# Performance work log

Hardware: AMD Instinct MI355X
Metric: run time of the kernel (lower is better)

Reference implementation:

```python
import jax, jax.numpy as jnp
import numpy as np

B, S, DIM = 2, 2048, 2048
H, KV = 16, 8
HD = DIM // H          # 128 head_dim
N_REP = H // KV        # 2


def _rope(x, cos, sin):
    # x: (B,S,h,HD) with interleaved (real, imag) pairs along last dim
    xr = x[..., 0::2]                      # (B,S,h,HD/2)
    xi = x[..., 1::2]
    cos = cos[None, :, None, :]            # (1,S,1,HD/2)
    sin = sin[None, :, None, :]
    or_ = xr * cos - xi * sin
    oi_ = xr * sin + xi * cos
    return jnp.stack([or_, oi_], axis=-1).reshape(x.shape)


def setup_inputs() -> dict:
    key = jax.random.key(0)
    ks = jax.random.split(key, 5)
    x = jax.random.normal(ks[0], (B, S, DIM), dtype=jnp.float32)
    # RoPE tables: theta = 10000, half = HD/2
    inv_freq = 1.0 / (10000.0 ** (np.arange(0, HD, 2, dtype=np.float32) / HD))
    t = np.arange(S, dtype=np.float32)
    ang = np.outer(t, inv_freq)                           # (S, HD/2)
    freqs_cos = jnp.asarray(np.cos(ang), dtype=jnp.float32)
    freqs_sin = jnp.asarray(np.sin(ang), dtype=jnp.float32)
    sc = 0.02
    wq = jax.random.normal(ks[1], (DIM, H * HD), dtype=jnp.float32) * sc
    wk = jax.random.normal(ks[2], (DIM, KV * HD), dtype=jnp.float32) * sc
    wv = jax.random.normal(ks[3], (DIM, KV * HD), dtype=jnp.float32) * sc
    wo = jax.random.normal(ks[4], (DIM, DIM), dtype=jnp.float32) * sc
    return {"x": x, "freqs_cos": freqs_cos, "freqs_sin": freqs_sin,
            "wq": wq, "wk": wk, "wv": wv, "wo": wo}


def reference(x, freqs_cos, freqs_sin, wq, wk, wv, wo):
    b, s, _ = x.shape
    xq = (x @ wq).reshape(b, s, H, HD)
    xk = (x @ wk).reshape(b, s, KV, HD)
    xv = (x @ wv).reshape(b, s, KV, HD)
    xq = _rope(xq, freqs_cos, freqs_sin)
    xk = _rope(xk, freqs_cos, freqs_sin)
    # GQA: repeat kv heads n_rep times along head axis
    xk = jnp.repeat(xk, N_REP, axis=2)     # (b,s,H,HD)
    xv = jnp.repeat(xv, N_REP, axis=2)
    scores = jnp.einsum('bqhd,bkhd->bhqk', xq, xk) / jnp.sqrt(
        jnp.asarray(HD, dtype=x.dtype))
    mask = jnp.triu(jnp.full((s, s), -jnp.inf, dtype=x.dtype), k=1)
    attn = jax.nn.softmax(scores + mask[None, None, :, :], axis=-1)
    out = jnp.einsum('bhqk,bkhd->bqhd', attn, xv).reshape(b, s, DIM)
    return out @ wo
```

## Files before the change

kernel.cpp:

```cpp
#include <hip/hip_runtime.h>

typedef unsigned short u16;
typedef short bf16x8 __attribute__((ext_vector_type(8)));
typedef float f32x4 __attribute__((ext_vector_type(4)));
typedef unsigned int u32x4 __attribute__((ext_vector_type(4)));
typedef unsigned short u16x4 __attribute__((ext_vector_type(4)));
typedef unsigned short u16x8 __attribute__((ext_vector_type(8)));

#define S_LEN 2048
#define NHEAD 16
#define NKV 8
#define HD 128

__device__ __forceinline__ u16 f2bf(float f) {
  unsigned u = __builtin_bit_cast(unsigned, f);
  u = (u + 0x7FFFu + ((u >> 16) & 1u)) >> 16;
  return (u16)u;
}
__device__ __forceinline__ float bf2f(u16 h) {
  unsigned u = ((unsigned)h) << 16;
  return __builtin_bit_cast(float, u);
}

__device__ __forceinline__ void gl_lds16(const void* g, void* l) {
  __builtin_amdgcn_global_load_lds(
      (const __attribute__((address_space(1))) unsigned int*)g,
      (__attribute__((address_space(3))) unsigned int*)l, 16, 0, 0);
}

__device__ __forceinline__ float redmax16(float v) {
  v = fmaxf(v, __shfl_xor(v, 1));
  v = fmaxf(v, __shfl_xor(v, 2));
  v = fmaxf(v, __shfl_xor(v, 4));
  v = fmaxf(v, __shfl_xor(v, 8));
  return v;
}

__global__ __launch_bounds__(256) void conv_bf16(const float* __restrict__ in,
                                                 u16* __restrict__ out, int n4) {
  int i = blockIdx.x * 256 + threadIdx.x;
  if (i >= n4) return;
  f32x4 v = *(const f32x4*)(in + (size_t)i * 4);
  u16x4 o;
#pragma unroll
  for (int j = 0; j < 4; ++j) o[j] = f2bf(v[j]);
  *(u16x4*)(out + (size_t)i * 4) = o;
}

__global__ __launch_bounds__(256) void transpose_w4(
    const float* __restrict__ wq, const float* __restrict__ wk,
    const float* __restrict__ wv, const float* __restrict__ wo,
    u16* __restrict__ wcatT, u16* __restrict__ woT) {
  __shared__ float tile[64][65];
  int id = blockIdx.x;
  const float* in;
  u16* out;
  int N, roff, nx;
  if (id < 1024) {
    in = wq; out = wcatT; N = 2048; roff = 0; nx = 32;
  } else if (id < 1536) {
    in = wk; out = wcatT; N = 1024; roff = 2048; nx = 16; id -= 1024;
  } else if (id < 2048) {
    in = wv; out = wcatT; N = 1024; roff = 3072; nx = 16; id -= 1536;
  } else {
    in = wo; out = woT; N = 2048; roff = 0; nx = 32; id -= 2048;
  }
  int bx = id % nx;
  int by = id / nx;
  int k0 = by * 64, n0 = bx * 64;
  int tx = threadIdx.x & 63, ty = threadIdx.x >> 6;
#pragma unroll
  for (int p = 0; p < 16; ++p) {
    int r = p * 4 + ty;
    tile[r][tx] = in[(size_t)(k0 + r) * N + n0 + tx];
  }
  __syncthreads();
#pragma unroll
  for (int p = 0; p < 16; ++p) {
    int r = p * 4 + ty;
    out[(size_t)(roff + n0 + r) * 2048 + k0 + tx] = f2bf(tile[tx][r]);
  }
}

__global__ __launch_bounds__(256) void rope_qk(u16* __restrict__ q, u16* __restrict__ k,
                                               const float* __restrict__ fc,
                                               const float* __restrict__ fs) {
  const int QC = 2 * NHEAD * S_LEN * HD / 8;
  const int KC = 2 * NKV * S_LEN * HD / 8;
  int i = blockIdx.x * 256 + threadIdx.x;
  if (i >= QC + KC) return;
  u16* base;
  float scale;
  size_t e;
  if (i < QC) {
    base = q;
    e = (size_t)i * 8;
    scale = 0.12751744540368598f;
  } else {
    base = k;
    e = (size_t)(i - QC) * 8;
    scale = 1.0f;
  }
  int d8 = (int)(e & 127);
  int s = (int)((e >> 7) & (S_LEN - 1));
  int dp0 = d8 >> 1;
  u16x8 v = *(const u16x8*)(base + e);
  u16x8 o;
#pragma unroll
  for (int p = 0; p < 4; ++p) {
    float xr = bf2f(v[2 * p]), xi = bf2f(v[2 * p + 1]);
    float c = fc[s * 64 + dp0 + p], sn = fs[s * 64 + dp0 + p];
    o[2 * p] = f2bf((xr * c - xi * sn) * scale);
    o[2 * p + 1] = f2bf((xr * sn + xi * c) * scale);
  }
  *(u16x8*)(base + e) = o;
}

template <int EPI>
__global__ __launch_bounds__(512, 1) void gemm3r(
    const u16* __restrict__ A, const u16* __restrict__ Bt, float* __restrict__ Cf,
    u16* __restrict__ Qo, u16* __restrict__ Ko, u16* __restrict__ Vo, int N, int ntn) {
  constexpr int K = 2048, NT = K / 64;
  constexpr int BSZ = (128 + 256) * 64;
  __shared__ __align__(16) u16 lds[3][BSZ];

  const int t = threadIdx.x;
  const int l = t & 63, lh = l >> 4, ll = l & 15;
  const int w = t >> 6, wm = w >> 2, wn = w & 3;

  const int bid = blockIdx.x;
  const int swz = (bid & 7) * (gridDim.x >> 3) + (bid >> 3);
  const int tm = swz / ntn, tn = swz % ntn;

  const u16* Ab = A + (size_t)tm * 128 * K;
  const u16* Bb = Bt + (size_t)tn * 256 * K;

  const int sr = t >> 3;
  const int sc8 = ((t & 7) ^ (sr & 7)) * 8;

  f32x4 acc[4][4] = {};

  auto STAGE = [&](int tau) {
    const int kt = tau * 64;
    u16* buf = &lds[tau % 3][0];
#pragma unroll
    for (int c = 0; c < 2; ++c)
      gl_lds16(Ab + (size_t)(c * 64 + sr) * K + kt + sc8, buf + c * 4096 + t * 8);
#pragma unroll
    for (int c = 0; c < 4; ++c)
      gl_lds16(Bb + (size_t)(c * 64 + sr) * K + kt + sc8,
               buf + 8192 + c * 4096 + t * 8);
  };

  STAGE(0);
  STAGE(1);
  __builtin_amdgcn_s_waitcnt(0xF70 | 6);
  __builtin_amdgcn_s_barrier();
  asm volatile("" ::: "memory");

  for (int tt = 0; tt < NT; ++tt) {
    if (tt + 2 < NT) STAGE(tt + 2);
    const u16* bufA = &lds[tt % 3][0];
    const u16* bufB = bufA + 8192;
#pragma unroll
    for (int kk = 0; kk < 2; ++kk) {
      const int cb = ((kk * 4 + lh) ^ (ll & 7)) * 8;
      bf16x8 af[4], bv[4];
#pragma unroll
      for (int m = 0; m < 4; ++m)
        af[m] = *(const bf16x8*)(bufA + (wm * 64 + m * 16 + ll) * 64 + cb);
#pragma unroll
      for (int n = 0; n < 4; ++n)
        bv[n] = *(const bf16x8*)(bufB + (wn * 64 + n * 16 + ll) * 64 + cb);
      __builtin_amdgcn_s_setprio(1);
#pragma unroll
      for (int m = 0; m < 4; ++m)
#pragma unroll
        for (int n = 0; n < 4; ++n)
          acc[m][n] =
              __builtin_amdgcn_mfma_f32_16x16x32_bf16(af[m], bv[n], acc[m][n], 0, 0, 0);
      __builtin_amdgcn_s_setprio(0);
    }
    if (tt + 1 < NT) {
      if (tt + 2 < NT)
        __builtin_amdgcn_s_waitcnt(0xF70 | 6);
      else
        __builtin_amdgcn_s_waitcnt(0xF70);
      __builtin_amdgcn_s_barrier();
      asm volatile("" ::: "memory");
    }
  }

#pragma unroll
  for (int m = 0; m < 4; ++m)
#pragma unroll
    for (int n = 0; n < 4; ++n)
#pragma unroll
      for (int j = 0; j < 4; ++j) {
        int row = tm * 128 + wm * 64 + m * 16 + lh * 4 + j;
        int col = tn * 256 + wn * 64 + n * 16 + ll;
        if constexpr (EPI == 0) {
          Cf[(size_t)row * N + col] = acc[m][n][j];
        } else {
          int b = row >> 11, s = row & (S_LEN - 1);
          u16 val = f2bf(acc[m][n][j]);
          int d = col & 127;
          if (col < 2048) {
            int hh = col >> 7;
            Qo[(((size_t)b * NHEAD + hh) * S_LEN + s) * HD + d] = val;
          } else if (col < 3072) {
            int kh = (col >> 7) & 7;
            Ko[(((size_t)b * NKV + kh) * S_LEN + s) * HD + d] = val;
          } else {
            int kh = (col >> 7) & 7;
            Vo[(((size_t)b * NKV + kh) * S_LEN + s) * HD + d] = val;
          }
        }
      }
}

__global__ __launch_bounds__(256) void transpose_v(const u16* __restrict__ V,
                                                   u16* __restrict__ Vt) {
  __shared__ u16 tile[64][72];
  int id = blockIdx.x;
  int bkv = id >> 6;
  int dt = (id >> 5) & 1;
  int st = id & 31;
  const u16* Vb = V + (size_t)bkv * S_LEN * HD;
  u16* Vo = Vt + (size_t)bkv * HD * S_LEN;
  int r = threadIdx.x >> 3, c8 = (threadIdx.x & 7) * 8;
#pragma unroll
  for (int it = 0; it < 2; ++it) {
    int rr = it * 32 + r;
    *(u16x8*)(&tile[rr][c8]) =
        *(const u16x8*)(Vb + (size_t)(st * 64 + rr) * HD + dt * 64 + c8);
  }
  __syncthreads();
#pragma unroll
  for (int it = 0; it < 2; ++it) {
    int rr = it * 32 + r;
    u16x8 o;
#pragma unroll
    for (int j = 0; j < 8; ++j) o[j] = tile[c8 + j][rr];
    *(u16x8*)(Vo + (size_t)(dt * 64 + rr) * S_LEN + st * 64 + c8) = o;
  }
}

__global__ __launch_bounds__(256) void attn_fwd(const u16* __restrict__ Q,
                                                const u16* __restrict__ Kh,
                                                const u16* __restrict__ Vt,
                                                u16* __restrict__ O) {
  __shared__ __align__(16) u16 Ks[64 * 136];
  __shared__ __align__(16) u16 Vs[128 * 72];
  __shared__ __align__(16) u16 Ps[4 * 16 * 64];

  const int t = threadIdx.x;
  const int w = t >> 6, l = t & 63, lh = l >> 4, ll = l & 15;
  const int bid = blockIdx.x;
  const int swzb = (bid & 7) * 64 + (bid >> 3);
  const int bh = swzb >> 4;
  const int pair = swzb & 15;
  const int b = bh >> 4, h = bh & 15;
  const int bkv = b * NKV + (h >> 1);

  const u16* Qb = Q + (size_t)bh * S_LEN * HD;
  const u16* Kb = Kh + (size_t)bkv * S_LEN * HD;
  const u16* Vb = Vt + (size_t)bkv * HD * S_LEN;

  const int krow = t >> 4, kcol = (t & 15) * 8;
  const int vrow = t >> 3, vcol = (t & 7) * 8;

  const bf16x8 vones = {0x3F80, 0x3F80, 0x3F80, 0x3F80, 0x3F80, 0x3F80, 0x3F80, 0x3F80};

  auto loadKV = [&](int tile, u32x4 (&kr)[4], u32x4 (&vr)[4]) {
    const int kv0 = tile * 64;
#pragma unroll
    for (int p = 0; p < 4; ++p)
      kr[p] = *(const u32x4*)(Kb + (size_t)(kv0 + p * 16 + krow) * HD + kcol);
#pragma unroll
    for (int p = 0; p < 4; ++p)
      vr[p] = *(const u32x4*)(Vb + (size_t)(p * 32 + vrow) * S_LEN + kv0 + vcol);
  };
  auto storeKV = [&](u32x4 (&kr)[4], u32x4 (&vr)[4]) {
#pragma unroll
    for (int p = 0; p < 4; ++p)
      *(u32x4*)(Ks + (p * 16 + krow) * 136 + kcol) = kr[p];
#pragma unroll
    for (int p = 0; p < 4; ++p)
      *(u32x4*)(Vs + (p * 32 + vrow) * 72 + vcol) = vr[p];
  };

  for (int hf = 0; hf < 2; ++hf) {
    const int qt = hf ? (31 - pair) : pair;
    const int q0 = qt * 64;

    bf16x8 qf[4];
    const int qrow = q0 + w * 16 + ll;
#pragma unroll
    for (int c = 0; c < 4; ++c)
      qf[c] = *(const bf16x8*)(Qb + (size_t)qrow * HD + c * 32 + lh * 8);

    f32x4 accO[8] = {};
    f32x4 accL = {0.f, 0.f, 0.f, 0.f};
    float mrow[4] = {-1e30f, -1e30f, -1e30f, -1e30f};

    u32x4 kr[4], vr[4];
    loadKV(0, kr, vr);
    storeKV(kr, vr);
    __syncthreads();

    const int nt = qt + 1;
    for (int tt = 0; tt < nt; ++tt) {
      if (tt + 1 < nt) loadKV(tt + 1, kr, vr);

      f32x4 sf[4];
#pragma unroll
      for (int f = 0; f < 4; ++f) {
        sf[f] = f32x4{0.f, 0.f, 0.f, 0.f};
#pragma unroll
        for (int c = 0; c < 4; ++c) {
          bf16x8 kf = *(const bf16x8*)(Ks + (f * 16 + ll) * 136 + c * 32 + lh * 8);
          sf[f] = __builtin_amdgcn_mfma_f32_16x16x32_bf16(qf[c], kf, sf[f], 0, 0, 0);
        }
      }

      if (tt == nt - 1) {
        const int kv0 = tt * 64;
#pragma unroll
        for (int f = 0; f < 4; ++f)
#pragma unroll
          for (int j = 0; j < 4; ++j) {
            int kvg = kv0 + f * 16 + ll;
            int qg = q0 + w * 16 + lh * 4 + j;
            if (kvg > qg) sf[f][j] = -1e30f;
          }
      }

      float corr[4];
#pragma unroll
      for (int j = 0; j < 4; ++j) {
        float mx = fmaxf(fmaxf(sf[0][j], sf[1][j]), fmaxf(sf[2][j], sf[3][j]));
        mx = redmax16(mx);
        float mnew = fmaxf(mrow[j], mx);
        corr[j] = __builtin_amdgcn_exp2f(mrow[j] - mnew);
        mrow[j] = mnew;
#pragma unroll
        for (int f = 0; f < 4; ++f) sf[f][j] = __builtin_amdgcn_exp2f(sf[f][j] - mnew);
      }
#pragma unroll
      for (int n = 0; n < 8; ++n)
#pragma unroll
        for (int j = 0; j < 4; ++j) accO[n][j] *= corr[j];
#pragma unroll
      for (int j = 0; j < 4; ++j) accL[j] *= corr[j];

      char* Pw = (char*)(Ps + w * 16 * 64);
#pragma unroll
      for (int f = 0; f < 4; ++f)
#pragma unroll
        for (int j = 0; j < 4; ++j) {
          int rr = lh * 4 + j, cc = f * 16 + ll;
          unsigned bo = (unsigned)(rr * 128 + cc * 2) ^ (unsigned)((rr & 7) << 4);
          *(u16*)(Pw + bo) = f2bf(sf[f][j]);
        }

#pragma unroll
      for (int kc = 0; kc < 2; ++kc) {
        unsigned bo =
            (unsigned)(ll * 128 + (kc * 32 + lh * 8) * 2) ^ (unsigned)((ll & 7) << 4);
        bf16x8 pf = *(const bf16x8*)(Pw + bo);
#pragma unroll
        for (int n = 0; n < 8; ++n) {
          bf16x8 vf = *(const bf16x8*)(Vs + (n * 16 + ll) * 72 + kc * 32 + lh * 8);
          accO[n] = __builtin_amdgcn_mfma_f32_16x16x32_bf16(pf, vf, accO[n], 0, 0, 0);
        }
        accL = __builtin_amdgcn_mfma_f32_16x16x32_bf16(pf, vones, accL, 0, 0, 0);
      }

      __syncthreads();
      if (tt + 1 < nt) storeKV(kr, vr);
      __syncthreads();
    }

    float inv[4];
#pragma unroll
    for (int j = 0; j < 4; ++j) inv[j] = 1.0f / accL[j];
    const size_t orow = (size_t)(b * S_LEN + q0 + w * 16 + lh * 4) * 2048 + h * HD;
#pragma unroll
    for (int n = 0; n < 8; ++n)
#pragma unroll
      for (int j = 0; j < 4; ++j)
        O[orow + (size_t)j * 2048 + n * 16 + ll] = f2bf(accO[n][j] * inv[j]);
  }
}

extern "C" void kernel_launch(void* const* d_in, const int* in_sizes, int n_in,
                              void* d_out, int out_size, void* d_ws, size_t ws_size,
                              hipStream_t stream) {
  (void)in_sizes;
  (void)n_in;
  (void)out_size;
  (void)ws_size;
  const float* x = (const float*)d_in[0];
  const float* fc = (const float*)d_in[1];
  const float* fs = (const float*)d_in[2];
  const float* wq = (const float*)d_in[3];
  const float* wk = (const float*)d_in[4];
  const float* wv = (const float*)d_in[5];
  const float* wo = (const float*)d_in[6];
  float* out = (float*)d_out;

  char* ws = (char*)d_ws;
  u16* wcatT = (u16*)ws;
  u16* vtb = (u16*)ws;
  u16* woT = (u16*)(ws + 16777216);
  u16* xo = (u16*)(ws + 25165824);
  u16* qb = (u16*)(ws + 41943040);
  u16* kb = (u16*)(ws + 58720256);
  u16* vb = (u16*)(ws + 67108864);

  conv_bf16<<<8192, 256, 0, stream>>>(x, xo, 2097152);
  transpose_w4<<<3072, 256, 0, stream>>>(wq, wk, wv, wo, wcatT, woT);

  gemm3r<1><<<512, 512, 0, stream>>>(xo, wcatT, nullptr, qb, kb, vb, 4096, 16);
  transpose_v<<<1024, 256, 0, stream>>>(vb, vtb);
  rope_qk<<<6144, 256, 0, stream>>>(qb, kb, fc, fs);
  attn_fwd<<<512, 256, 0, stream>>>(qb, kb, vtb, xo);
  gemm3r<0><<<256, 512, 0, stream>>>(xo, woT, out, nullptr, nullptr, nullptr, 2048, 8);
}
```

Before: 233.3 us.

## Split KV loop across two wave groups in attention with LDS merge

The attention block grows to 512 threads: two groups of four waves each take alternating KV tiles for the same 64 query rows, and their partial softmax states (max, sum, output) are merged through shared memory at the end. K and V tiles move to an XOR-swizzled, unpadded LDS layout instead of padded rows. The aim is more in-flight waves and shorter serial KV chains per block. In exchange it adds a combine step, extra barriers and more LDS use, and an idle half when the tile count is odd.

Measured after the change: 329.5 us. +41.2%, slower.

```diff
diff --git a/kernel.cpp b/kernel.cpp
--- a/kernel.cpp
+++ b/kernel.cpp
@@ -246,16 +246,17 @@
   }
 }
 
-__global__ __launch_bounds__(256) void attn_fwd(const u16* __restrict__ Q,
-                                                const u16* __restrict__ Kh,
-                                                const u16* __restrict__ Vt,
-                                                u16* __restrict__ O) {
-  __shared__ __align__(16) u16 Ks[64 * 136];
-  __shared__ __align__(16) u16 Vs[128 * 72];
-  __shared__ __align__(16) u16 Ps[4 * 16 * 64];
+__global__ __launch_bounds__(512, 4) void attn_fwd(const u16* __restrict__ Q,
+                                                   const u16* __restrict__ Kh,
+                                                   const u16* __restrict__ Vt,
+                                                   u16* __restrict__ O) {
+  __shared__ __align__(16) u16 SH[40960];
 
   const int t = threadIdx.x;
   const int w = t >> 6, l = t & 63, lh = l >> 4, ll = l & 15;
+  const int qg = w & 3, half = w >> 2;
+  const int t256 = t & 255;
+
   const int bid = blockIdx.x;
   const int swzb = (bid & 7) * 64 + (bid >> 3);
   const int bh = swzb >> 4;
@@ -267,130 +268,188 @@
   const u16* Kb = Kh + (size_t)bkv * S_LEN * HD;
   const u16* Vb = Vt + (size_t)bkv * HD * S_LEN;
 
-  const int krow = t >> 4, kcol = (t & 15) * 8;
-  const int vrow = t >> 3, vcol = (t & 7) * 8;
+  u16* KS = SH + half * 8192;
+  u16* VS = SH + 16384 + half * 8192;
+  u16* PW = SH + 32768 + w * 1024;
+  float* CmbO = (float*)SH;
+  float* CmbML = (float*)(SH + 16384);
+
+  const int krow = t256 >> 4;
+  const int ksHi = t256 & 8, ksLo = t256 & 7;
+  const int vrow = t256 >> 3;
+  const int vsLo = t256 & 7;
+
+  u16x8 krg[4], vrg[4];
+  auto loadK = [&](int tile) {
+    const int kv0 = tile * 64;
+#pragma unroll
+    for (int p = 0; p < 4; ++p) {
+      int r = p * 16 + krow;
+      int s = ksHi | (ksLo ^ (r & 7));
+      krg[p] = *(const u16x8*)(Kb + (size_t)(kv0 + r) * HD + s * 8);
+    }
+  };
+  auto loadV = [&](int tile) {
+    const int kv0 = tile * 64;
+#pragma unroll
+    for (int i = 0; i < 4; ++i) {
+      int d = i * 32 + vrow;
+      int s = vsLo ^ (d & 7);
+      vrg[i] = *(const u16x8*)(Vb + (size_t)d * S_LEN + kv0 + s * 8);
+    }
+  };
+  auto storeKV = [&]() {
+#pragma unroll
+    for (int p = 0; p < 4; ++p)
+      *(u16x8*)(KS + (p * 16 + krow) * 128 + (t256 & 15) * 8) = krg[p];
+#pragma unroll
+    for (int i = 0; i < 4; ++i)
+      *(u16x8*)(VS + (i * 32 + vrow) * 64 + vsLo * 8) = vrg[i];
+  };
 
   const bf16x8 vones = {0x3F80, 0x3F80, 0x3F80, 0x3F80, 0x3F80, 0x3F80, 0x3F80, 0x3F80};
-
-  auto loadKV = [&](int tile, u32x4 (&kr)[4], u32x4 (&vr)[4]) {
-    const int kv0 = tile * 64;
-#pragma unroll
-    for (int p = 0; p < 4; ++p)
-      kr[p] = *(const u32x4*)(Kb + (size_t)(kv0 + p * 16 + krow) * HD + kcol);
-#pragma unroll
-    for (int p = 0; p < 4; ++p)
-      vr[p] = *(const u32x4*)(Vb + (size_t)(p * 32 + vrow) * S_LEN + kv0 + vcol);
-  };
-  auto storeKV = [&](u32x4 (&kr)[4], u32x4 (&vr)[4]) {
-#pragma unroll
-    for (int p = 0; p < 4; ++p)
-      *(u32x4*)(Ks + (p * 16 + krow) * 136 + kcol) = kr[p];
-#pragma unroll
-    for (int p = 0; p < 4; ++p)
-      *(u32x4*)(Vs + (p * 32 + vrow) * 72 + vcol) = vr[p];
-  };
 
   for (int hf = 0; hf < 2; ++hf) {
     const int qt = hf ? (31 - pair) : pair;
     const int q0 = qt * 64;
 
     bf16x8 qf[4];
-    const int qrow = q0 + w * 16 + ll;
 #pragma unroll
     for (int c = 0; c < 4; ++c)
-      qf[c] = *(const bf16x8*)(Qb + (size_t)qrow * HD + c * 32 + lh * 8);
+      qf[c] = *(const bf16x8*)(Qb + (size_t)(q0 + qg * 16 + ll) * HD + c * 32 + lh * 8);
 
     f32x4 accO[8] = {};
     f32x4 accL = {0.f, 0.f, 0.f, 0.f};
     float mrow[4] = {-1e30f, -1e30f, -1e30f, -1e30f};
 
-    u32x4 kr[4], vr[4];
-    loadKV(0, kr, vr);
-    storeKV(kr, vr);
+    const int nt = qt + 1;
+    const int nt2 = (nt + 1) >> 1;
+    int ti = half;
+    if (ti < nt) {
+      loadK(ti);
+      loadV(ti);
+    }
     __syncthreads();
-
-    const int nt = qt + 1;
-    for (int tt = 0; tt < nt; ++tt) {
-      if (tt + 1 < nt) loadKV(tt + 1, kr, vr);
+    if (ti < nt) storeKV();
+    __syncthreads();
+
+    for (int i = 0; i < nt2; ++i) {
+      const int tin = ti + 2;
+      const bool act = ti < nt;
+      const bool actn = tin < nt;
+      if (actn) loadK(tin);
 
       f32x4 sf[4];
-#pragma unroll
-      for (int f = 0; f < 4; ++f) {
-        sf[f] = f32x4{0.f, 0.f, 0.f, 0.f};
-#pragma unroll
-        for (int c = 0; c < 4; ++c) {
-          bf16x8 kf = *(const bf16x8*)(Ks + (f * 16 + ll) * 136 + c * 32 + lh * 8);
-          sf[f] = __builtin_amdgcn_mfma_f32_16x16x32_bf16(qf[c], kf, sf[f], 0, 0, 0);
+      if (act) {
+#pragma unroll
+        for (int f = 0; f < 4; ++f) {
+          sf[f] = f32x4{0.f, 0.f, 0.f, 0.f};
+#pragma unroll
+          for (int c = 0; c < 4; ++c) {
+            const int slot = c * 4 + lh;
+            const int eff = (slot & 8) | ((slot & 7) ^ (ll & 7));
+            bf16x8 kf = *(const bf16x8*)(KS + (f * 16 + ll) * 128 + eff * 8);
+            sf[f] = __builtin_amdgcn_mfma_f32_16x16x32_bf16(qf[c], kf, sf[f], 0, 0, 0);
+          }
+        }
+        if (ti == nt - 1) {
+          const int kv0 = ti * 64;
+#pragma unroll
+          for (int f = 0; f < 4; ++f)
+#pragma unroll
+            for (int j = 0; j < 4; ++j) {
+              int kvg = kv0 + f * 16 + ll;
+              int qgl = q0 + qg * 16 + lh * 4 + j;
+              if (kvg > qgl) sf[f][j] = -1e30f;
+            }
         }
       }
-
-      if (tt == nt - 1) {
-        const int kv0 = tt * 64;
+      if (actn) loadV(tin);
+      if (act) {
+        float corr[4];
+#pragma unroll
+        for (int j = 0; j < 4; ++j) {
+          float mx = fmaxf(fmaxf(sf[0][j], sf[1][j]), fmaxf(sf[2][j], sf[3][j]));
+          mx = redmax16(mx);
+          float mnew = fmaxf(mrow[j], mx);
+          corr[j] = __builtin_amdgcn_exp2f(mrow[j] - mnew);
+          mrow[j] = mnew;
+#pragma unroll
+          for (int f = 0; f < 4; ++f) sf[f][j] = __builtin_amdgcn_exp2f(sf[f][j] - mnew);
+        }
+#pragma unroll
+        for (int n = 0; n < 8; ++n)
+#pragma unroll
+          for (int j = 0; j < 4; ++j) accO[n][j] *= corr[j];
+#pragma unroll
+        for (int j = 0; j < 4; ++j) accL[j] *= corr[j];
+
+        char* Pw = (char*)PW;
 #pragma unroll
         for (int f = 0; f < 4; ++f)
 #pragma unroll
           for (int j = 0; j < 4; ++j) {
-            int kvg = kv0 + f * 16 + ll;
-            int qg = q0 + w * 16 + lh * 4 + j;
-            if (kvg > qg) sf[f][j] = -1e30f;
+            int rr = lh * 4 + j, cc = f * 16 + ll;
+            unsigned bo = (unsigned)(rr * 128 + cc * 2) ^ (unsigned)((rr & 7) << 4);
+            *(u16*)(Pw + bo) = f2bf(sf[f][j]);
           }
+
+#pragma unroll
+        for (int kc = 0; kc < 2; ++kc) {
+          unsigned bo =
+              (unsigned)(ll * 128 + (kc * 32 + lh * 8) * 2) ^ (unsigned)((ll & 7) << 4);
+          bf16x8 pf = *(const bf16x8*)(Pw + bo);
+#pragma unroll
+          for (int n = 0; n < 8; ++n) {
+            const int eff = (kc * 4 + lh) ^ (ll & 7);
+            bf16x8 vf = *(const bf16x8*)(VS + (n * 16 + ll) * 64 + eff * 8);
+            accO[n] = __builtin_amdgcn_mfma_f32_16x16x32_bf16(pf, vf, accO[n], 0, 0, 0);
+          }
+          accL = __builtin_amdgcn_mfma_f32_16x16x32_bf16(pf, vones, accL, 0, 0, 0);
+        }
       }
-
-      float corr[4];
+      __syncthreads();
+      if (actn) storeKV();
+      __syncthreads();
+      ti = tin;
+    }
+
+    if (half == 1) {
+#pragma unroll
+      for (int n = 0; n < 8; ++n)
+#pragma unroll
+        for (int j = 0; j < 4; ++j)
+          CmbO[(qg * 16 + lh * 4 + j) * 128 + n * 16 + ll] = accO[n][j];
+      if (ll == 0) {
+#pragma unroll
+        for (int j = 0; j < 4; ++j) {
+          CmbML[qg * 32 + lh * 4 + j] = mrow[j];
+          CmbML[qg * 32 + 16 + lh * 4 + j] = accL[j];
+        }
+      }
+    }
+    __syncthreads();
+    if (half == 0) {
+      float aa[4], bb[4], inv[4];
 #pragma unroll
       for (int j = 0; j < 4; ++j) {
-        float mx = fmaxf(fmaxf(sf[0][j], sf[1][j]), fmaxf(sf[2][j], sf[3][j]));
-        mx = redmax16(mx);
-        float mnew = fmaxf(mrow[j], mx);
-        corr[j] = __builtin_amdgcn_exp2f(mrow[j] - mnew);
-        mrow[j] = mnew;
-#pragma unroll
-        for (int f = 0; f < 4; ++f) sf[f][j] = __builtin_amdgcn_exp2f(sf[f][j] - mnew);
+        float m2 = CmbML[qg * 32 + lh * 4 + j];
+        float l2 = CmbML[qg * 32 + 16 + lh * 4 + j];
+        float mf = fmaxf(mrow[j], m2);
+        aa[j] = __builtin_amdgcn_exp2f(mrow[j] - mf);
+        bb[j] = __builtin_amdgcn_exp2f(m2 - mf);
+        inv[j] = 1.0f / (accL[j] * aa[j] + l2 * bb[j]);
       }
+      const size_t orow = (size_t)(b * S_LEN + q0 + qg * 16 + lh * 4) * 2048 + h * HD;
 #pragma unroll
       for (int n = 0; n < 8; ++n)
 #pragma unroll
-        for (int j = 0; j < 4; ++j) accO[n][j] *= corr[j];
-#pragma unroll
-      for (int j = 0; j < 4; ++j) accL[j] *= corr[j];
-
-      char* Pw = (char*)(Ps + w * 16 * 64);
-#pragma unroll
-      for (int f = 0; f < 4; ++f)
-#pragma unroll
         for (int j = 0; j < 4; ++j) {
-          int rr = lh * 4 + j, cc = f * 16 + ll;
-          unsigned bo = (unsigned)(rr * 128 + cc * 2) ^ (unsigned)((rr & 7) << 4);
-          *(u16*)(Pw + bo) = f2bf(sf[f][j]);
-        }
-
-#pragma unroll
-      for (int kc = 0; kc < 2; ++kc) {
-        unsigned bo =
-            (unsigned)(ll * 128 + (kc * 32 + lh * 8) * 2) ^ (unsigned)((ll & 7) << 4);
-        bf16x8 pf = *(const bf16x8*)(Pw + bo);
-#pragma unroll
-        for (int n = 0; n < 8; ++n) {
-          bf16x8 vf = *(const bf16x8*)(Vs + (n * 16 + ll) * 72 + kc * 32 + lh * 8);
-          accO[n] = __builtin_amdgcn_mfma_f32_16x16x32_bf16(pf, vf, accO[n], 0, 0, 0);
-        }
-        accL = __builtin_amdgcn_mfma_f32_16x16x32_bf16(pf, vones, accL, 0, 0, 0);
-      }
-
-      __syncthreads();
-      if (tt + 1 < nt) storeKV(kr, vr);
-      __syncthreads();
-    }
-
-    float inv[4];
-#pragma unroll
-    for (int j = 0; j < 4; ++j) inv[j] = 1.0f / accL[j];
-    const size_t orow = (size_t)(b * S_LEN + q0 + w * 16 + lh * 4) * 2048 + h * HD;
-#pragma unroll
-    for (int n = 0; n < 8; ++n)
-#pragma unroll
-      for (int j = 0; j < 4; ++j)
-        O[orow + (size_t)j * 2048 + n * 16 + ll] = f2bf(accO[n][j] * inv[j]);
+          float o2 = CmbO[(qg * 16 + lh * 4 + j) * 128 + n * 16 + ll];
+          O[orow + (size_t)j * 2048 + n * 16 + ll] =
+              f2bf((accO[n][j] * aa[j] + o2 * bb[j]) * inv[j]);
+        }
+    }
   }
 }
 
@@ -425,6 +484,6 @@
   gemm3r<1><<<512, 512, 0, stream>>>(xo, wcatT, nullptr, qb, kb, vb, 4096, 16);
   transpose_v<<<1024, 256, 0, stream>>>(vb, vtb);
   rope_qk<<<6144, 256, 0, stream>>>(qb, kb, fc, fs);
-  attn_fwd<<<512, 256, 0, stream>>>(qb, kb, vtb, xo);
+  attn_fwd<<<512, 512, 0, stream>>>(qb, kb, vtb, xo);
   gemm3r<0><<<256, 512, 0, stream>>>(xo, woT, out, nullptr, nullptr, nullptr, 2048, 8);
 }
```

## Rewrite attention kernel with 32x32 MFMA, transposed scores and lazy rescaling

Applied to the files above, without the earlier changes.

Rewrites the flash-attention kernel to use 32x32x16 bf16 MFMA. It computes S^T so that each lane owns one query row, which makes the row max and sum register-local. P is repacked with permlane32_swap instead of going through LDS. K and V tiles are double-buffered in XOR-swizzled LDS, 128-query tiles replace the paired 64-row tiles, and the output is only rescaled when the max grows by more than a threshold. This cuts LDS traffic, shuffles and per-tile rescaling, at the cost of more registers and a different load-balancing scheme (no pair folding, heavy tiles scheduled first).

Measured after the change: 212.3 us. 9.0% less time.

```diff
diff --git a/kernel.cpp b/kernel.cpp
--- a/kernel.cpp
+++ b/kernel.cpp
@@ -3,6 +3,8 @@
 typedef unsigned short u16;
 typedef short bf16x8 __attribute__((ext_vector_type(8)));
 typedef float f32x4 __attribute__((ext_vector_type(4)));
+typedef float f32x16 __attribute__((ext_vector_type(16)));
+typedef int i32x2 __attribute__((ext_vector_type(2)));
 typedef unsigned int u32x4 __attribute__((ext_vector_type(4)));
 typedef unsigned short u16x4 __attribute__((ext_vector_type(4)));
 typedef unsigned short u16x8 __attribute__((ext_vector_type(8)));
@@ -28,12 +30,10 @@
       (__attribute__((address_space(3))) unsigned int*)l, 16, 0, 0);
 }
 
-__device__ __forceinline__ float redmax16(float v) {
-  v = fmaxf(v, __shfl_xor(v, 1));
-  v = fmaxf(v, __shfl_xor(v, 2));
-  v = fmaxf(v, __shfl_xor(v, 4));
-  v = fmaxf(v, __shfl_xor(v, 8));
-  return v;
+__device__ __forceinline__ unsigned cvtpk_bf16(float a, float b) {
+  unsigned r;
+  asm("v_cvt_pk_bf16_f32 %0, %1, %2" : "=v"(r) : "v"(a), "v"(b));
+  return r;
 }
 
 __global__ __launch_bounds__(256) void conv_bf16(const float* __restrict__ in,
@@ -246,20 +246,20 @@
   }
 }
 
-__global__ __launch_bounds__(256) void attn_fwd(const u16* __restrict__ Q,
-                                                const u16* __restrict__ Kh,
-                                                const u16* __restrict__ Vt,
-                                                u16* __restrict__ O) {
-  __shared__ __align__(16) u16 Ks[64 * 136];
-  __shared__ __align__(16) u16 Vs[128 * 72];
-  __shared__ __align__(16) u16 Ps[4 * 16 * 64];
+__global__ __launch_bounds__(256, 2) void attn_fwd(const u16* __restrict__ Q,
+                                                   const u16* __restrict__ Kh,
+                                                   const u16* __restrict__ Vt,
+                                                   u16* __restrict__ O) {
+  __shared__ __align__(16) u16 KS[2][64 * 128];
+  __shared__ __align__(16) u16 VS[2][128 * 64];
 
   const int t = threadIdx.x;
-  const int w = t >> 6, l = t & 63, lh = l >> 4, ll = l & 15;
+  const int l = t & 63, hi = l >> 5, ll = l & 31;
+  const int wq = t >> 6;
+
   const int bid = blockIdx.x;
-  const int swzb = (bid & 7) * 64 + (bid >> 3);
-  const int bh = swzb >> 4;
-  const int pair = swzb & 15;
+  const int qt = 15 - (bid >> 5);
+  const int bh = bid & 31;
   const int b = bh >> 4, h = bh & 15;
   const int bkv = b * NKV + (h >> 1);
 
@@ -267,131 +267,181 @@
   const u16* Kb = Kh + (size_t)bkv * S_LEN * HD;
   const u16* Vb = Vt + (size_t)bkv * HD * S_LEN;
 
-  const int krow = t >> 4, kcol = (t & 15) * 8;
-  const int vrow = t >> 3, vcol = (t & 7) * 8;
-
-  const bf16x8 vones = {0x3F80, 0x3F80, 0x3F80, 0x3F80, 0x3F80, 0x3F80, 0x3F80, 0x3F80};
-
-  auto loadKV = [&](int tile, u32x4 (&kr)[4], u32x4 (&vr)[4]) {
+  const int q0w = qt * 128 + wq * 32;
+  const int qg = q0w + ll;
+
+  bf16x8 qf[8];
+#pragma unroll
+  for (int c = 0; c < 8; ++c)
+    qf[c] = *(const bf16x8*)(Qb + (size_t)qg * HD + c * 16 + hi * 8);
+
+  const int krow = t >> 4, kslot = t & 15;
+  const int vrow = t >> 3, vslot = t & 7;
+  u16x8 krg[4], vrg[4];
+
+  auto loadKV = [&](int tile) {
     const int kv0 = tile * 64;
 #pragma unroll
-    for (int p = 0; p < 4; ++p)
-      kr[p] = *(const u32x4*)(Kb + (size_t)(kv0 + p * 16 + krow) * HD + kcol);
-#pragma unroll
-    for (int p = 0; p < 4; ++p)
-      vr[p] = *(const u32x4*)(Vb + (size_t)(p * 32 + vrow) * S_LEN + kv0 + vcol);
+    for (int c = 0; c < 4; ++c) {
+      int r = c * 16 + krow;
+      int sg = (kslot & 8) | ((kslot & 7) ^ (r & 7));
+      krg[c] = *(const u16x8*)(Kb + (size_t)(kv0 + r) * HD + sg * 8);
+    }
+#pragma unroll
+    for (int c = 0; c < 4; ++c) {
+      int d = c * 32 + vrow;
+      int sg = vslot ^ (d & 7);
+      vrg[c] = *(const u16x8*)(Vb + (size_t)d * S_LEN + kv0 + sg * 8);
+    }
   };
-  auto storeKV = [&](u32x4 (&kr)[4], u32x4 (&vr)[4]) {
-#pragma unroll
-    for (int p = 0; p < 4; ++p)
-      *(u32x4*)(Ks + (p * 16 + krow) * 136 + kcol) = kr[p];
-#pragma unroll
-    for (int p = 0; p < 4; ++p)
-      *(u32x4*)(Vs + (p * 32 + vrow) * 72 + vcol) = vr[p];
+  auto storeKV = [&](int bi) {
+#pragma unroll
+    for (int c = 0; c < 4; ++c)
+      *(u16x8*)(&KS[bi][(c * 16 + krow) * 128 + kslot * 8]) = krg[c];
+#pragma unroll
+    for (int c = 0; c < 4; ++c)
+      *(u16x8*)(&VS[bi][(c * 32 + vrow) * 64 + vslot * 8]) = vrg[c];
   };
 
-  for (int hf = 0; hf < 2; ++hf) {
-    const int qt = hf ? (31 - pair) : pair;
-    const int q0 = qt * 64;
-
-    bf16x8 qf[4];
-    const int qrow = q0 + w * 16 + ll;
-#pragma unroll
-    for (int c = 0; c < 4; ++c)
-      qf[c] = *(const bf16x8*)(Qb + (size_t)qrow * HD + c * 32 + lh * 8);
-
-    f32x4 accO[8] = {};
-    f32x4 accL = {0.f, 0.f, 0.f, 0.f};
-    float mrow[4] = {-1e30f, -1e30f, -1e30f, -1e30f};
-
-    u32x4 kr[4], vr[4];
-    loadKV(0, kr, vr);
-    storeKV(kr, vr);
-    __syncthreads();
-
-    const int nt = qt + 1;
-    for (int tt = 0; tt < nt; ++tt) {
-      if (tt + 1 < nt) loadKV(tt + 1, kr, vr);
-
-      f32x4 sf[4];
-#pragma unroll
-      for (int f = 0; f < 4; ++f) {
-        sf[f] = f32x4{0.f, 0.f, 0.f, 0.f};
-#pragma unroll
-        for (int c = 0; c < 4; ++c) {
-          bf16x8 kf = *(const bf16x8*)(Ks + (f * 16 + ll) * 136 + c * 32 + lh * 8);
-          sf[f] = __builtin_amdgcn_mfma_f32_16x16x32_bf16(qf[c], kf, sf[f], 0, 0, 0);
+  f32x16 accO[4] = {};
+  float m = -1e30f, lsum = 0.f;
+
+  const int nt = 2 * qt + 2;
+  loadKV(0);
+  storeKV(0);
+  __syncthreads();
+
+  for (int tt = 0; tt < nt; ++tt) {
+    const int kv0 = tt * 64;
+    const bool actn = (tt + 1 < nt);
+    if (actn) loadKV(tt + 1);
+
+    if (kv0 <= q0w + 31) {
+      const u16* ks = &KS[tt & 1][0];
+      const u16* vs = &VS[tt & 1][0];
+
+      f32x16 st[2] = {};
+      __builtin_amdgcn_s_setprio(1);
+#pragma unroll
+      for (int c = 0; c < 8; ++c) {
+        int slot = 2 * c + hi;
+        int eff = (slot & 8) | ((slot & 7) ^ (ll & 7));
+        bf16x8 kf0 = *(const bf16x8*)(ks + (size_t)ll * 128 + eff * 8);
+        st[0] = __builtin_amdgcn_mfma_f32_32x32x16_bf16(kf0, qf[c], st[0], 0, 0, 0);
+        bf16x8 kf1 = *(const bf16x8*)(ks + (size_t)(32 + ll) * 128 + eff * 8);
+        st[1] = __builtin_amdgcn_mfma_f32_32x32x16_bf16(kf1, qf[c], st[1], 0, 0, 0);
+      }
+      __builtin_amdgcn_s_setprio(0);
+
+      if (kv0 + 63 > q0w) {
+#pragma unroll
+        for (int f = 0; f < 2; ++f)
+#pragma unroll
+          for (int r = 0; r < 16; ++r) {
+            int kvg = kv0 + f * 32 + (r & 3) + 8 * (r >> 2) + 4 * hi;
+            if (kvg > qg) st[f][r] = -1e30f;
+          }
+      }
+
+      float a[16];
+#pragma unroll
+      for (int i = 0; i < 16; ++i) a[i] = fmaxf(st[0][i], st[1][i]);
+#pragma unroll
+      for (int s = 8; s >= 1; s >>= 1)
+#pragma unroll
+        for (int i = 0; i < 8; ++i)
+          if (i < s) a[i] = fmaxf(a[i], a[i + s]);
+      float pmax = fmaxf(a[0], __shfl_xor(a[0], 32));
+
+      if (tt == 0) {
+        m = pmax;
+      } else if (!__all(pmax <= m + 8.0f)) {
+        float mnew = fmaxf(m, pmax);
+        float corr = __builtin_amdgcn_exp2f(m - mnew);
+        m = mnew;
+        lsum *= corr;
+        int ci = __builtin_bit_cast(int, corr);
+#pragma unroll
+        for (int reg = 0; reg < 16; ++reg) {
+          int row = (reg & 3) + 8 * (reg >> 2) + 4 * hi;
+          float cq = __builtin_bit_cast(
+              float, __builtin_amdgcn_ds_bpermute(row << 2, ci));
+#pragma unroll
+          for (int dblk = 0; dblk < 4; ++dblk) accO[dblk][reg] *= cq;
         }
       }
 
-      if (tt == nt - 1) {
-        const int kv0 = tt * 64;
-#pragma unroll
-        for (int f = 0; f < 4; ++f)
-#pragma unroll
-          for (int j = 0; j < 4; ++j) {
-            int kvg = kv0 + f * 16 + ll;
-            int qg = q0 + w * 16 + lh * 4 + j;
-            if (kvg > qg) sf[f][j] = -1e30f;
-          }
+#pragma unroll
+      for (int f = 0; f < 2; ++f)
+#pragma unroll
+        for (int r = 0; r < 16; ++r)
+          st[f][r] = __builtin_amdgcn_exp2f(st[f][r] - m);
+      float s1[16];
+#pragma unroll
+      for (int i = 0; i < 16; ++i) s1[i] = st[0][i] + st[1][i];
+#pragma unroll
+      for (int s = 8; s >= 1; s >>= 1)
+#pragma unroll
+        for (int i = 0; i < 8; ++i)
+          if (i < s) s1[i] += s1[i + s];
+      lsum += s1[0];
+
+      unsigned pk[8][2];
+#pragma unroll
+      for (int bg = 0; bg < 8; ++bg)
+#pragma unroll
+        for (int ap = 0; ap < 2; ++ap)
+          pk[bg][ap] = cvtpk_bf16(st[bg >> 2][(bg & 3) * 4 + 2 * ap],
+                                  st[bg >> 2][(bg & 3) * 4 + 2 * ap + 1]);
+
+      __builtin_amdgcn_s_setprio(1);
+#pragma unroll
+      for (int kc = 0; kc < 4; ++kc) {
+        i32x2 sa = __builtin_amdgcn_permlane32_swap(
+            (int)pk[2 * kc][0], (int)pk[2 * kc + 1][0], false, false);
+        i32x2 sb = __builtin_amdgcn_permlane32_swap(
+            (int)pk[2 * kc][1], (int)pk[2 * kc + 1][1], false, false);
+        union {
+          unsigned u[4];
+          bf16x8 v;
+        } pa;
+        pa.u[0] = (unsigned)sa[0];
+        pa.u[1] = (unsigned)sb[0];
+        pa.u[2] = (unsigned)sa[1];
+        pa.u[3] = (unsigned)sb[1];
+        int eff = (2 * kc + hi) ^ (ll & 7);
+#pragma unroll
+        for (int dblk = 0; dblk < 4; ++dblk) {
+          bf16x8 vf = *(const bf16x8*)(vs + (size_t)(dblk * 32 + ll) * 64 + eff * 8);
+          accO[dblk] =
+              __builtin_amdgcn_mfma_f32_32x32x16_bf16(pa.v, vf, accO[dblk], 0, 0, 0);
+        }
       }
-
-      float corr[4];
-#pragma unroll
-      for (int j = 0; j < 4; ++j) {
-        float mx = fmaxf(fmaxf(sf[0][j], sf[1][j]), fmaxf(sf[2][j], sf[3][j]));
-        mx = redmax16(mx);
-        float mnew = fmaxf(mrow[j], mx);
-        corr[j] = __builtin_amdgcn_exp2f(mrow[j] - mnew);
-        mrow[j] = mnew;
-#pragma unroll
-        for (int f = 0; f < 4; ++f) sf[f][j] = __builtin_amdgcn_exp2f(sf[f][j] - mnew);
-      }
-#pragma unroll
-      for (int n = 0; n < 8; ++n)
-#pragma unroll
-        for (int j = 0; j < 4; ++j) accO[n][j] *= corr[j];
-#pragma unroll
-      for (int j = 0; j < 4; ++j) accL[j] *= corr[j];
-
-      char* Pw = (char*)(Ps + w * 16 * 64);
-#pragma unroll
-      for (int f = 0; f < 4; ++f)
-#pragma unroll
-        for (int j = 0; j < 4; ++j) {
-          int rr = lh * 4 + j, cc = f * 16 + ll;
-          unsigned bo = (unsigned)(rr * 128 + cc * 2) ^ (unsigned)((rr & 7) << 4);
-          *(u16*)(Pw + bo) = f2bf(sf[f][j]);
-        }
-
-#pragma unroll
-      for (int kc = 0; kc < 2; ++kc) {
-        unsigned bo =
-            (unsigned)(ll * 128 + (kc * 32 + lh * 8) * 2) ^ (unsigned)((ll & 7) << 4);
-        bf16x8 pf = *(const bf16x8*)(Pw + bo);
-#pragma unroll
-        for (int n = 0; n < 8; ++n) {
-          bf16x8 vf = *(const bf16x8*)(Vs + (n * 16 + ll) * 72 + kc * 32 + lh * 8);
-          accO[n] = __builtin_amdgcn_mfma_f32_16x16x32_bf16(pf, vf, accO[n], 0, 0, 0);
-        }
-        accL = __builtin_amdgcn_mfma_f32_16x16x32_bf16(pf, vones, accL, 0, 0, 0);
-      }
-
-      __syncthreads();
-      if (tt + 1 < nt) storeKV(kr, vr);
-      __syncthreads();
-    }
-
-    float inv[4];
-#pragma unroll
-    for (int j = 0; j < 4; ++j) inv[j] = 1.0f / accL[j];
-    const size_t orow = (size_t)(b * S_LEN + q0 + w * 16 + lh * 4) * 2048 + h * HD;
-#pragma unroll
-    for (int n = 0; n < 8; ++n)
-#pragma unroll
-      for (int j = 0; j < 4; ++j)
-        O[orow + (size_t)j * 2048 + n * 16 + ll] = f2bf(accO[n][j] * inv[j]);
-  }
+      __builtin_amdgcn_s_setprio(0);
+    }
+
+    __syncthreads();
+    if (actn) storeKV((tt + 1) & 1);
+    __syncthreads();
+  }
+
+  lsum += __shfl_xor(lsum, 32);
+  float linv = 1.0f / lsum;
+  int li = __builtin_bit_cast(int, linv);
+  float inv[16];
+#pragma unroll
+  for (int reg = 0; reg < 16; ++reg) {
+    int row = (reg & 3) + 8 * (reg >> 2) + 4 * hi;
+    inv[reg] = __builtin_bit_cast(float, __builtin_amdgcn_ds_bpermute(row << 2, li));
+  }
+#pragma unroll
+  for (int dblk = 0; dblk < 4; ++dblk)
+#pragma unroll
+    for (int reg = 0; reg < 16; ++reg) {
+      int row = (reg & 3) + 8 * (reg >> 2) + 4 * hi;
+      O[(size_t)(b * S_LEN + q0w + row) * 2048 + h * HD + dblk * 32 + ll] =
+          f2bf(accO[dblk][reg] * inv[reg]);
+    }
 }
 
 extern "C" void kernel_launch(void* const* d_in, const int* in_sizes, int n_in,
```
